# Kernel optimization log

Measured on AMD Instinct MI355X. Metric: run time of the kernel, lower is better.

Reference implementation:

```python
import jax, jax.numpy as jnp
import numpy as np

B, N, CS = 4, 384, 384
CZ = 128
H, C, PQ, PV = 12, 16, 4, 8
INF, EPS = 1e5, 1e-8


def _rigid_apply(rot, trans, pts):
    # rot: [B,N,3,3], trans: [B,N,3], pts: [B,N,P,3]
    return jnp.einsum('bnij,bnpj->bnpi', rot, pts) + trans[:, :, None, :]


def _pts_from_linear(x, n_pts):
    # torch: split last dim into 3 chunks (x,y,z blocks) then stack on dim -1
    Bx, Nx = x.shape[:2]
    return jnp.moveaxis(x.reshape(Bx, Nx, 3, n_pts), -2, -1)  # [B,N,n_pts,3]


def _forward(s, z, rot, trans, mask, w_q, b_q, w_kv, b_kv, w_gq, b_gq, w_gk, b_gk,
             w_qp, b_qp, w_kvp, b_kvp, head_weights, w_out, b_out):
    del z  # z is an unused arg in the original forward
    Bx, Nx, _ = s.shape
    q = (s @ w_q + b_q).reshape(Bx, Nx, H, C)
    kv = (s @ w_kv + b_kv).reshape(Bx, Nx, H, 2 * C)
    k, v = kv[..., :C], kv[..., C:]
    # g_q / g_k are computed in the original but never used (dead code):
    _ = (s.sum(0) @ w_gq + b_gq)
    _ = (s.sum(0) @ w_gk + b_gk)

    q_pts = _pts_from_linear(s @ w_qp + b_qp, H * PQ)
    q_pts = _rigid_apply(rot, trans, q_pts).reshape(Bx, Nx, H, PQ, 3)
    kv_pts = _pts_from_linear(s @ w_kvp + b_kvp, H * (PQ + PV))
    kv_pts = _rigid_apply(rot, trans, kv_pts).reshape(Bx, Nx, H, PQ + PV, 3)
    k_pts, v_pts = kv_pts[..., :PQ, :], kv_pts[..., PQ:, :]

    scale = np.sqrt(1.0 / (3 * C)).astype(np.float32)
    a = jnp.einsum('bihc,bjhc->bhij', q, k) * scale  # [B,H,N,N]
    a_g = a  # original recomputes the identical q@k product

    # point-distance attention bias; diff is [B,N,N,H,PQ,3]
    diff = q_pts[:, :, None] - k_pts[:, None]
    sq = jnp.sum(diff * diff, axis=-1)  # [B,N,N,H,PQ]
    hw = jax.nn.softplus(head_weights) * np.sqrt(1.0 / (3 * (PQ * 9.0 / 2))).astype(np.float32)
    pt_att = -0.5 * jnp.sum(sq * hw[:, None], axis=-1)  # [B,N,N,H]
    pt_att = jnp.moveaxis(pt_att, -1, 1)  # [B,H,N,N]

    square_mask = INF * (mask[:, :, None] * mask[:, None, :] - 1.0)  # [B,N,N]
    a = jax.nn.softmax(a + square_mask[:, None] + a_g + pt_att, axis=-1)

    o = jnp.einsum('bhij,bjhc->bihc', a, v).reshape(Bx, Nx, H * C)
    o_pt = jnp.einsum('bhij,bjhpx->bihpx', a, v_pts)  # [B,N,H,PV,3]
    # invert_apply: rot^T (x - t)
    o_pt = jnp.einsum('bnji,bnhpj->bnhpi', rot, o_pt - trans[:, :, None, None, :])
    o_pt_norm = jnp.sqrt(jnp.sum(o_pt ** 2, axis=-1) + EPS).reshape(Bx, Nx, H * PV)
    o_pt = o_pt.reshape(Bx, Nx, H * PV, 3)
    cat = jnp.concatenate([o, o_pt[..., 0], o_pt[..., 1], o_pt[..., 2], o_pt_norm], axis=-1)
    return cat @ w_out + b_out


def setup_inputs() -> dict:
    key = jax.random.key(0)
    ks = jax.random.split(key, 16)
    lin = lambda k, fi, fo: jax.random.normal(k, (fi, fo), jnp.float32) / np.sqrt(fi).astype(np.float32)
    hc = H * C
    out_dim = H * (C + PV * 4)
    return {
        's': jax.random.normal(ks[0], (B, N, CS), jnp.float32),
        'z': jax.random.normal(ks[1], (B, N, N, CZ), jnp.float32),
        'rot': jnp.linalg.qr(jax.random.normal(ks[2], (B, N, 3, 3), jnp.float32))[0],
        'trans': jax.random.normal(ks[3], (B, N, 3), jnp.float32),
        'mask': jnp.ones((B, N), jnp.float32),
        'w_q': lin(ks[4], CS, hc), 'b_q': jnp.zeros((hc,), jnp.float32),
        'w_kv': lin(ks[5], CS, 2 * hc), 'b_kv': jnp.zeros((2 * hc,), jnp.float32),
        'w_gq': lin(ks[6], CS, hc), 'b_gq': jnp.zeros((hc,), jnp.float32),
        'w_gk': lin(ks[7], CS, hc), 'b_gk': jnp.zeros((hc,), jnp.float32),
        'w_qp': lin(ks[8], CS, H * PQ * 3), 'b_qp': jnp.zeros((H * PQ * 3,), jnp.float32),
        'w_kvp': lin(ks[9], CS, H * (PQ + PV) * 3), 'b_kvp': jnp.zeros((H * (PQ + PV) * 3,), jnp.float32),
        'head_weights': jnp.full((H,), 0.541324854, jnp.float32),  # softplus^-1(1)
        'w_out': lin(ks[10], out_dim, CS), 'b_out': jnp.zeros((CS,), jnp.float32),
    }


def reference(s, z, rot, trans, mask, w_q, b_q, w_kv, b_kv, w_gq, b_gq, w_gk, b_gk,
              w_qp, b_qp, w_kvp, b_kvp, head_weights, w_out, b_out):
    return _forward(s, z, rot, trans, mask, w_q, b_q, w_kv, b_kv, w_gq, b_gq, w_gk, b_gk,
                    w_qp, b_qp, w_kvp, b_kvp, head_weights, w_out, b_out)
```

## Files before the change

### kernel.cpp

```cpp
#include <hip/hip_runtime.h>
#include <math.h>

#define Bb 4
#define Nn 384
#define CSs 384
#define Hh 12
#define Cc 16
#define PQq 4
#define PVv 8
#define FPROJ 1152
#define FCAT 576
#define INFV 100000.0f
#define EPSV 1e-8f

#define WS_PROJ 0
#define WS_CAT  3022848
#define WS_PART 4423680
#define PSTRIDE 2688
#define WS_WT   9068544
#define WS_WTO  9289728
#define WS_AH   9400320
#define WS_AL   9695232
#define WS_KH   9990144
#define WS_KL   10285056
#define WS_VBP  10579968

typedef __attribute__((ext_vector_type(8))) short short8v;
typedef __attribute__((ext_vector_type(4))) float f32x4;

__device__ __forceinline__ short f2bf(float x) {
    unsigned u = __float_as_uint(x);
    unsigned r = (u + 0x7FFFu + ((u >> 16) & 1u)) >> 16;
    return (short)r;
}
__device__ __forceinline__ float bf2f(short h) {
    return __uint_as_float(((unsigned)(unsigned short)h) << 16);
}

__device__ __forceinline__ float get_bias(int f,
    const float* __restrict__ b_q, const float* __restrict__ b_kv,
    const float* __restrict__ b_qp, const float* __restrict__ b_kvp)
{
    if (f < 192) return b_q[f];
    if (f < 576) return b_kv[f - 192];
    if (f < 720) return b_qp[f - 576];
    return b_kvp[f - 720];
}

__global__ __launch_bounds__(256) void prep_kernel(
    const float* __restrict__ w_q, const float* __restrict__ w_kv,
    const float* __restrict__ w_qp, const float* __restrict__ w_kvp,
    const float* __restrict__ w_out,
    short* __restrict__ wt, short* __restrict__ wto)
{
    int idx = blockIdx.x * 256 + threadIdx.x;
    if (idx < 1152 * 384) {
        int f = idx / 384, k = idx % 384;
        float v;
        if (f < 192)      v = w_q[(size_t)k * 192 + f];
        else if (f < 576) v = w_kv[(size_t)k * 384 + (f - 192)];
        else if (f < 720) v = w_qp[(size_t)k * 144 + (f - 576)];
        else              v = w_kvp[(size_t)k * 432 + (f - 720)];
        wt[idx] = f2bf(v);
    } else if (idx < 1152 * 384 + 384 * 576) {
        int j = idx - 1152 * 384;
        int f = j / 576, k = j % 576;
        wto[j] = f2bf(w_out[(size_t)k * 384 + f]);
    }
}

__global__ __launch_bounds__(256) void proj_kernel(
    const float* __restrict__ s, const short* __restrict__ wt,
    const float* __restrict__ b_q, const float* __restrict__ b_kv,
    const float* __restrict__ b_qp, const float* __restrict__ b_kvp,
    float* __restrict__ proj)
{
    __shared__ short Al[64 * 40];
    __shared__ short Bl[64 * 40];

    const int bm = blockIdx.x % 24;
    const int bn = blockIdx.x / 24;
    const int m0 = bm * 64;
    const int f0 = bn * 64;
    const int t = threadIdx.x;
    const int w = t >> 6;
    const int lane = t & 63;
    const int lrow = lane & 15;
    const int lkg  = lane >> 4;

    const int srow = t >> 2;
    const int sseg = t & 3;

    f32x4 acc0 = {0,0,0,0}, acc1 = {0,0,0,0}, acc2 = {0,0,0,0}, acc3 = {0,0,0,0};

    for (int ks = 0; ks < 12; ++ks) {
        const int kbase = ks * 32;
        {
            const float* sp = s + (size_t)(m0 + srow) * CSs + kbase + sseg * 8;
            float4 v0 = *(const float4*)sp;
            float4 v1 = *(const float4*)(sp + 4);
            short8v a;
            a[0]=f2bf(v0.x); a[1]=f2bf(v0.y); a[2]=f2bf(v0.z); a[3]=f2bf(v0.w);
            a[4]=f2bf(v1.x); a[5]=f2bf(v1.y); a[6]=f2bf(v1.z); a[7]=f2bf(v1.w);
            *(short8v*)&Al[srow * 40 + sseg * 8] = a;
        }
        {
            short8v bvv = *(const short8v*)&wt[(size_t)(f0 + srow) * 384 + kbase + sseg * 8];
            *(short8v*)&Bl[srow * 40 + sseg * 8] = bvv;
        }
        __syncthreads();

        short8v av = *(const short8v*)&Al[(16 * w + lrow) * 40 + lkg * 8];
        short8v b0 = *(const short8v*)&Bl[(lrow) * 40 + lkg * 8];
        short8v b1 = *(const short8v*)&Bl[(16 + lrow) * 40 + lkg * 8];
        short8v b2 = *(const short8v*)&Bl[(32 + lrow) * 40 + lkg * 8];
        short8v b3 = *(const short8v*)&Bl[(48 + lrow) * 40 + lkg * 8];
        acc0 = __builtin_amdgcn_mfma_f32_16x16x32_bf16(av, b0, acc0, 0, 0, 0);
        acc1 = __builtin_amdgcn_mfma_f32_16x16x32_bf16(av, b1, acc1, 0, 0, 0);
        acc2 = __builtin_amdgcn_mfma_f32_16x16x32_bf16(av, b2, acc2, 0, 0, 0);
        acc3 = __builtin_amdgcn_mfma_f32_16x16x32_bf16(av, b3, acc3, 0, 0, 0);
        __syncthreads();
    }

    const int orow = m0 + 16 * w + lkg * 4;
#pragma unroll
    for (int e = 0; e < 4; ++e) {
        float* pr = proj + (size_t)(orow + e) * FPROJ + f0;
        int c0 = lrow;
        pr[c0]      = acc0[e] + get_bias(f0 + c0,      b_q, b_kv, b_qp, b_kvp);
        pr[16 + c0] = acc1[e] + get_bias(f0 + 16 + c0, b_q, b_kv, b_qp, b_kvp);
        pr[32 + c0] = acc2[e] + get_bias(f0 + 32 + c0, b_q, b_kv, b_qp, b_kvp);
        pr[48 + c0] = acc3[e] + get_bias(f0 + 48 + c0, b_q, b_kv, b_qp, b_kvp);
    }
}

__global__ __launch_bounds__(192) void pack_kernel(
    const float* __restrict__ proj,
    const float* __restrict__ rot, const float* __restrict__ trans,
    const float* __restrict__ hwts, const float* __restrict__ mask,
    short* __restrict__ Ah, short* __restrict__ Al,
    short* __restrict__ Kh, short* __restrict__ Kl,
    short* __restrict__ Vbp)
{
    __shared__ float abuf[12 * 32];
    __shared__ float kbuf[12 * 32];
    __shared__ float vbuf[12 * 40];
    __shared__ float kpsq[12 * 4];

    const int bn = blockIdx.x;
    const int b = bn / Nn;
    const int n = bn % Nn;
    const int t = threadIdx.x;
    const float* R = rot + (size_t)bn * 9;
    const float* T = trans + (size_t)bn * 3;
    const float* pr = proj + (size_t)bn * FPROJ;
    const float mi = mask[bn];

    if (t < 144) {
        float x = pr[720 + t];
        float y = pr[720 + 144 + t];
        float z = pr[720 + 288 + t];
        float ox = R[0]*x + R[1]*y + R[2]*z + T[0];
        float oy = R[3]*x + R[4]*y + R[5]*z + T[1];
        float oz = R[6]*x + R[7]*y + R[8]*z + T[2];
        int h = t / 12, pp = t % 12;
        if (pp < PQq) {
            kbuf[h*32 + 16 + pp*3 + 0] = ox;
            kbuf[h*32 + 16 + pp*3 + 1] = oy;
            kbuf[h*32 + 16 + pp*3 + 2] = oz;
            kpsq[h*4 + pp] = ox*ox + oy*oy + oz*oz;
        } else {
            vbuf[h*40 + 16 + (pp - PQq)*3 + 0] = ox;
            vbuf[h*40 + 16 + (pp - PQq)*3 + 1] = oy;
            vbuf[h*40 + 16 + (pp - PQq)*3 + 2] = oz;
        }
    }
    if (t < 48) {
        float x = pr[576 + t];
        float y = pr[576 + 48 + t];
        float z = pr[576 + 96 + t];
        float ox = R[0]*x + R[1]*y + R[2]*z + T[0];
        float oy = R[3]*x + R[4]*y + R[5]*z + T[1];
        float oz = R[6]*x + R[7]*y + R[8]*z + T[2];
        int h = t / 4, p = t % 4;
        float n2wc = log1pf(expf(hwts[h])) * 0.13608276348795434f;
        abuf[h*32 + 16 + p*3 + 0] = n2wc * ox;
        abuf[h*32 + 16 + p*3 + 1] = n2wc * oy;
        abuf[h*32 + 16 + p*3 + 2] = n2wc * oz;
    }
    {
        int h = t >> 4, c = t & 15;
        abuf[h*32 + c] = 0.28867513459481287f * pr[h * 16 + c];
        kbuf[h*32 + c] = pr[192 + h * 32 + c];
        vbuf[h*40 + c] = pr[192 + h * 32 + 16 + c];
    }
    if (t < 12) {
        abuf[t*32 + 28] = 1.0f;  abuf[t*32 + 29] = mi;
        abuf[t*32 + 30] = 0.0f;  abuf[t*32 + 31] = 0.0f;
        kbuf[t*32 + 29] = INFV * (mi - 1.0f);
        kbuf[t*32 + 30] = 0.0f;  kbuf[t*32 + 31] = 0.0f;
    }
    __syncthreads();
    if (t < 12) {
        float hw2 = log1pf(expf(hwts[t]));
        float wc = -0.5f * hw2 * 0.13608276348795434f;
        kbuf[t*32 + 28] = wc * (kpsq[t*4] + kpsq[t*4+1] + kpsq[t*4+2] + kpsq[t*4+3]);
    }
    __syncthreads();

    if (t < 48) {
        int h = t >> 2, pc = t & 3;
        const float* src = &abuf[h*32 + pc*8];
        short8v hi, lo;
#pragma unroll
        for (int k = 0; k < 8; ++k) {
            short hh = f2bf(src[k]);
            hi[k] = hh; lo[k] = f2bf(src[k] - bf2f(hh));
        }
        size_t off = ((size_t)((b * Hh + h) * Nn + n)) * 32 + pc * 8;
        *(short8v*)&Ah[off] = hi;
        *(short8v*)&Al[off] = lo;
    } else if (t < 96) {
        int tt = t - 48, h = tt >> 2, pc = tt & 3;
        const float* src = &kbuf[h*32 + pc*8];
        short8v hi, lo;
#pragma unroll
        for (int k = 0; k < 8; ++k) {
            short hh = f2bf(src[k]);
            hi[k] = hh; lo[k] = f2bf(src[k] - bf2f(hh));
        }
        size_t off = ((size_t)((b * Hh + h) * Nn + n)) * 32 + pc * 8;
        *(short8v*)&Kh[off] = hi;
        *(short8v*)&Kl[off] = lo;
    } else if (t < 156) {
        int tt = t - 96, h = tt / 5, pc = tt % 5;
        const float* src = &vbuf[h*40 + pc*8];
        short8v v;
#pragma unroll
        for (int k = 0; k < 8; ++k) v[k] = f2bf(src[k]);
        *(short8v*)&Vbp[((size_t)((b * Hh + h) * Nn + n)) * 40 + pc * 8] = v;
    }
}

__global__ __launch_bounds__(256) void attn_part_kernel(
    const short* __restrict__ Ah, const short* __restrict__ Al,
    const short* __restrict__ Kh, const short* __restrict__ Kl,
    const short* __restrict__ Vbp,
    float* __restrict__ part)
{
    __shared__ short smem_s[13696];
    short* Ahi = smem_s;
    short* Alo = smem_s + 2560;
    short* Khi = smem_s + 5120;
    short* Klo = smem_s + 7680;
    short* Vb  = smem_s + 10240;
    short* Pb  = smem_s;

    const int bid = blockIdx.x;
    const int jc = bid % 6;
    const int ic = (bid / 6) % 6;
    const int h  = (bid / 36) % Hh;
    const int b  = bid / (36 * Hh);
    const int t  = threadIdx.x;
    const int i0 = ic * 64;
    const int j0 = jc * 64;
    const int bh = b * Hh + h;

    const short* AhB = Ah + ((size_t)(bh * Nn + i0)) * 32;
    const short* AlB = Al + ((size_t)(bh * Nn + i0)) * 32;
    const short* KhB = Kh + ((size_t)(bh * Nn + j0)) * 32;
    const short* KlB = Kl + ((size_t)(bh * Nn + j0)) * 32;
    const short* VbB = Vbp + ((size_t)(bh * Nn + j0)) * 40;

    {
        const int i = t >> 2, pc = t & 3;
        *(short8v*)&Ahi[i * 40 + pc * 8] = *(const short8v*)&AhB[i * 32 + pc * 8];
        *(short8v*)&Alo[i * 40 + pc * 8] = *(const short8v*)&AlB[i * 32 + pc * 8];
        *(short8v*)&Khi[i * 40 + pc * 8] = *(const short8v*)&KhB[i * 32 + pc * 8];
        *(short8v*)&Klo[i * 40 + pc * 8] = *(const short8v*)&KlB[i * 32 + pc * 8];
    }
#pragma unroll
    for (int e = t; e < 320; e += 256) {
        int j = e / 5, pc = e % 5;
        short8v v = *(const short8v*)&VbB[j * 40 + pc * 8];
#pragma unroll
        for (int k = 0; k < 8; ++k) Vb[(pc * 8 + k) * 72 + j] = v[k];
    }
    if (t < 144) {
        int o = 40 * 72 + t * 4;
        Vb[o] = 0; Vb[o+1] = 0; Vb[o+2] = 0; Vb[o+3] = 0;
    }
    __syncthreads();

    const int w = t >> 6;
    const int lane = t & 63;
    const int lrow = lane & 15;
    const int lkg  = lane >> 4;

    f32x4 La0 = {0,0,0,0}, La1 = {0,0,0,0}, La2 = {0,0,0,0}, La3 = {0,0,0,0};
    {
        short8v ahi = *(const short8v*)&Ahi[(16 * w + lrow) * 40 + lkg * 8];
        short8v alo = *(const short8v*)&Alo[(16 * w + lrow) * 40 + lkg * 8];
        short8v k0h = *(const short8v*)&Khi[(lrow) * 40 + lkg * 8];
        short8v k1h = *(const short8v*)&Khi[(16 + lrow) * 40 + lkg * 8];
        short8v k2h = *(const short8v*)&Khi[(32 + lrow) * 40 + lkg * 8];
        short8v k3h = *(const short8v*)&Khi[(48 + lrow) * 40 + lkg * 8];
        short8v k0l = *(const short8v*)&Klo[(lrow) * 40 + lkg * 8];
        short8v k1l = *(const short8v*)&Klo[(16 + lrow) * 40 + lkg * 8];
        short8v k2l = *(const short8v*)&Klo[(32 + lrow) * 40 + lkg * 8];
        short8v k3l = *(const short8v*)&Klo[(48 + lrow) * 40 + lkg * 8];
        La0 = __builtin_amdgcn_mfma_f32_16x16x32_bf16(ahi, k0h, La0, 0, 0, 0);
        La1 = __builtin_amdgcn_mfma_f32_16x16x32_bf16(ahi, k1h, La1, 0, 0, 0);
        La2 = __builtin_amdgcn_mfma_f32_16x16x32_bf16(ahi, k2h, La2, 0, 0, 0);
        La3 = __builtin_amdgcn_mfma_f32_16x16x32_bf16(ahi, k3h, La3, 0, 0, 0);
        La0 = __builtin_amdgcn_mfma_f32_16x16x32_bf16(alo, k0h, La0, 0, 0, 0);
        La1 = __builtin_amdgcn_mfma_f32_16x16x32_bf16(alo, k1h, La1, 0, 0, 0);
        La2 = __builtin_amdgcn_mfma_f32_16x16x32_bf16(alo, k2h, La2, 0, 0, 0);
        La3 = __builtin_amdgcn_mfma_f32_16x16x32_bf16(alo, k3h, La3, 0, 0, 0);
        La0 = __builtin_amdgcn_mfma_f32_16x16x32_bf16(ahi, k0l, La0, 0, 0, 0);
        La1 = __builtin_amdgcn_mfma_f32_16x16x32_bf16(ahi, k1l, La1, 0, 0, 0);
        La2 = __builtin_amdgcn_mfma_f32_16x16x32_bf16(ahi, k2l, La2, 0, 0, 0);
        La3 = __builtin_amdgcn_mfma_f32_16x16x32_bf16(ahi, k3l, La3, 0, 0, 0);
    }

    const size_t pidx = ((size_t)(bh * 6 + ic)) * 6 + jc;
    float* po = part + pidx * PSTRIDE;

    float m0_, m1_, m2_, m3_, s0_, s1_, s2_, s3_;
    float p00,p10,p20,p30, p01,p11,p21,p31, p02,p12,p22,p32, p03,p13,p23,p33;

#define SMAX_E(E, TM, SM, P0, P1, P2, P3) { \
    float tmax_ = fmaxf(fmaxf(La0[E], La1[E]), fmaxf(La2[E], La3[E])); \
    tmax_ = fmaxf(tmax_, __shfl_xor(tmax_, 1)); \
    tmax_ = fmaxf(tmax_, __shfl_xor(tmax_, 2)); \
    tmax_ = fmaxf(tmax_, __shfl_xor(tmax_, 4)); \
    tmax_ = fmaxf(tmax_, __shfl_xor(tmax_, 8)); \
    P0 = __expf(La0[E] - tmax_); P1 = __expf(La1[E] - tmax_); \
    P2 = __expf(La2[E] - tmax_); P3 = __expf(La3[E] - tmax_); \
    float cs_ = P0 + P1 + P2 + P3; \
    cs_ += __shfl_xor(cs_, 1); cs_ += __shfl_xor(cs_, 2); \
    cs_ += __shfl_xor(cs_, 4); cs_ += __shfl_xor(cs_, 8); \
    TM = tmax_; SM = cs_; }

    SMAX_E(0, m0_, s0_, p00, p10, p20, p30);
    SMAX_E(1, m1_, s1_, p01, p11, p21, p31);
    SMAX_E(2, m2_, s2_, p02, p12, p22, p32);
    SMAX_E(3, m3_, s3_, p03, p13, p23, p33);
#undef SMAX_E

    if (lrow == 0) {
        int rb = 16 * w + 4 * lkg;
        po[2560 + rb + 0] = m0_; po[2624 + rb + 0] = s0_;
        po[2560 + rb + 1] = m1_; po[2624 + rb + 1] = s1_;
        po[2560 + rb + 2] = m2_; po[2624 + rb + 2] = s2_;
        po[2560 + rb + 3] = m3_; po[2624 + rb + 3] = s3_;
    }
    __syncthreads();

#define PW(E, PJ0, PJ1, PJ2, PJ3) { \
    int r_ = (16 * w + 4 * lkg + E) * 72; \
    Pb[r_ + lrow]      = f2bf(PJ0); \
    Pb[r_ + 16 + lrow] = f2bf(PJ1); \
    Pb[r_ + 32 + lrow] = f2bf(PJ2); \
    Pb[r_ + 48 + lrow] = f2bf(PJ3); }
    PW(0, p00, p10, p20, p30);
    PW(1, p01, p11, p21, p31);
    PW(2, p02, p12, p22, p32);
    PW(3, p03, p13, p23, p33);
#undef PW
    __syncthreads();

    f32x4 O0 = {0,0,0,0}, O1 = {0,0,0,0}, O2 = {0,0,0,0};
#pragma unroll
    for (int ch = 0; ch < 2; ++ch) {
        short8v pf = *(const short8v*)&Pb[(16 * w + lrow) * 72 + ch * 32 + lkg * 8];
        short8v v0 = *(const short8v*)&Vb[(lrow) * 72 + ch * 32 + lkg * 8];
        short8v v1 = *(const short8v*)&Vb[(16 + lrow) * 72 + ch * 32 + lkg * 8];
        short8v v2 = *(const short8v*)&Vb[(32 + lrow) * 72 + ch * 32 + lkg * 8];
        O0 = __builtin_amdgcn_mfma_f32_16x16x32_bf16(pf, v0, O0, 0, 0, 0);
        O1 = __builtin_amdgcn_mfma_f32_16x16x32_bf16(pf, v1, O1, 0, 0, 0);
        O2 = __builtin_amdgcn_mfma_f32_16x16x32_bf16(pf, v2, O2, 0, 0, 0);
    }
#pragma unroll
    for (int e = 0; e < 4; ++e) {
        int r = 16 * w + 4 * lkg + e;
        po[r * 40 + lrow]      = O0[e];
        po[r * 40 + 16 + lrow] = O1[e];
        if (lrow < 8) po[r * 40 + 32 + lrow] = O2[e];
    }
}

__global__ __launch_bounds__(256) void attn_merge_kernel(
    const float* __restrict__ part,
    const float* __restrict__ rot, const float* __restrict__ trans,
    short* __restrict__ cat_bf)
{
    __shared__ float wsh[64 * 8];
    __shared__ float ob[64 * 44];

    const int bid = blockIdx.x;
    const int ic = bid % 6;
    const int h  = (bid / 6) % Hh;
    const int b  = bid / (6 * Hh);
    const int t  = threadIdx.x;
    const int i0 = ic * 64;
    const int bh = b * Hh + h;
    const size_t pbase = (((size_t)(bh * 6 + ic)) * 6) * PSTRIDE;

    if (t < 64) {
        float mk[6], sk[6];
        float M = -3.0e38f;
#pragma unroll
        for (int k = 0; k < 6; ++k) {
            mk[k] = part[pbase + (size_t)k * PSTRIDE + 2560 + t];
            sk[k] = part[pbase + (size_t)k * PSTRIDE + 2624 + t];
            M = fmaxf(M, mk[k]);
        }
        float wk[6]; float stot = 0.0f;
#pragma unroll
        for (int k = 0; k < 6; ++k) {
            wk[k] = __expf(mk[k] - M);
            stot += wk[k] * sk[k];
        }
        float inv = 1.0f / stot;
#pragma unroll
        for (int k = 0; k < 6; ++k) wsh[t * 8 + k] = wk[k] * inv;
    }
    __syncthreads();

#pragma unroll
    for (int it = 0; it < 10; ++it) {
        int idx = t + it * 256;
        int row = idx / 40, col = idx % 40;
        float v = 0.0f;
#pragma unroll
        for (int k = 0; k < 6; ++k)
            v += wsh[row * 8 + k] * part[pbase + (size_t)k * PSTRIDE + row * 40 + col];
        ob[row * 44 + col] = v;
    }
    __syncthreads();

    {
        const int i = t >> 2;
        const int qq = t & 3;
        const int bnI = b * Nn + i0 + i;
        short* crow = cat_bf + (size_t)bnI * FCAT;

        float4 o = *(const float4*)&ob[i * 44 + 4 * qq];
        crow[h * 16 + 4 * qq + 0] = f2bf(o.x);
        crow[h * 16 + 4 * qq + 1] = f2bf(o.y);
        crow[h * 16 + 4 * qq + 2] = f2bf(o.z);
        crow[h * 16 + 4 * qq + 3] = f2bf(o.w);

        const float* R = rot + (size_t)bnI * 9;
        const float* T = trans + (size_t)bnI * 3;
#pragma unroll
        for (int e = 0; e < 2; ++e) {
            int pe = qq + 4 * e;
            float g0 = ob[i * 44 + 16 + 3 * pe + 0] - T[0];
            float g1 = ob[i * 44 + 16 + 3 * pe + 1] - T[1];
            float g2 = ob[i * 44 + 16 + 3 * pe + 2] - T[2];
            float lx = R[0]*g0 + R[3]*g1 + R[6]*g2;
            float ly = R[1]*g0 + R[4]*g1 + R[7]*g2;
            float lz = R[2]*g0 + R[5]*g1 + R[8]*g2;
            crow[192 + h * 8 + pe] = f2bf(lx);
            crow[288 + h * 8 + pe] = f2bf(ly);
            crow[384 + h * 8 + pe] = f2bf(lz);
            crow[480 + h * 8 + pe] = f2bf(sqrtf(lx*lx + ly*ly + lz*lz + EPSV));
        }
    }
}

__global__ __launch_bounds__(256) void out_kernel(
    const short* __restrict__ cat_bf, const short* __restrict__ wto,
    const float* __restrict__ b_out, float* __restrict__ out)
{
    __shared__ short Al[64 * 40];
    __shared__ short Bl[64 * 40];

    const int bm = blockIdx.x % 24;
    const int bn = blockIdx.x / 24;
    const int m0 = bm * 64;
    const int n0 = bn * 64;
    const int t = threadIdx.x;
    const int w = t >> 6;
    const int lane = t & 63;
    const int lrow = lane & 15;
    const int lkg  = lane >> 4;

    const int srow = t >> 2;
    const int sseg = t & 3;

    f32x4 acc0 = {0,0,0,0}, acc1 = {0,0,0,0}, acc2 = {0,0,0,0}, acc3 = {0,0,0,0};

    for (int ks = 0; ks < 18; ++ks) {
        const int kbase = ks * 32;
        {
            short8v a = *(const short8v*)&cat_bf[(size_t)(m0 + srow) * FCAT + kbase + sseg * 8];
            *(short8v*)&Al[srow * 40 + sseg * 8] = a;
        }
        {
            short8v bvv = *(const short8v*)&wto[(size_t)(n0 + srow) * FCAT + kbase + sseg * 8];
            *(short8v*)&Bl[srow * 40 + sseg * 8] = bvv;
        }
        __syncthreads();

        short8v av = *(const short8v*)&Al[(16 * w + lrow) * 40 + lkg * 8];
        short8v b0 = *(const short8v*)&Bl[(lrow) * 40 + lkg * 8];
        short8v b1 = *(const short8v*)&Bl[(16 + lrow) * 40 + lkg * 8];
        short8v b2 = *(const short8v*)&Bl[(32 + lrow) * 40 + lkg * 8];
        short8v b3 = *(const short8v*)&Bl[(48 + lrow) * 40 + lkg * 8];
        acc0 = __builtin_amdgcn_mfma_f32_16x16x32_bf16(av, b0, acc0, 0, 0, 0);
        acc1 = __builtin_amdgcn_mfma_f32_16x16x32_bf16(av, b1, acc1, 0, 0, 0);
        acc2 = __builtin_amdgcn_mfma_f32_16x16x32_bf16(av, b2, acc2, 0, 0, 0);
        acc3 = __builtin_amdgcn_mfma_f32_16x16x32_bf16(av, b3, acc3, 0, 0, 0);
        __syncthreads();
    }

    const int orow = m0 + 16 * w + lkg * 4;
#pragma unroll
    for (int e = 0; e < 4; ++e) {
        float* pr = out + (size_t)(orow + e) * 384 + n0;
        int c0 = lrow;
        pr[c0]      = acc0[e] + b_out[n0 + c0];
        pr[16 + c0] = acc1[e] + b_out[n0 + 16 + c0];
        pr[32 + c0] = acc2[e] + b_out[n0 + 32 + c0];
        pr[48 + c0] = acc3[e] + b_out[n0 + 48 + c0];
    }
}

extern "C" void kernel_launch(void* const* d_in, const int* in_sizes, int n_in,
                              void* d_out, int out_size, void* d_ws, size_t ws_size,
                              hipStream_t stream) {
    const float* s     = (const float*)d_in[0];
    const float* rot   = (const float*)d_in[2];
    const float* trans = (const float*)d_in[3];
    const float* mask  = (const float*)d_in[4];
    const float* w_q   = (const float*)d_in[5];
    const float* b_q   = (const float*)d_in[6];
    const float* w_kv  = (const float*)d_in[7];
    const float* b_kv  = (const float*)d_in[8];
    const float* w_qp  = (const float*)d_in[13];
    const float* b_qp  = (const float*)d_in[14];
    const float* w_kvp = (const float*)d_in[15];
    const float* b_kvp = (const float*)d_in[16];
    const float* hwts  = (const float*)d_in[17];
    const float* w_out = (const float*)d_in[18];
    const float* b_out = (const float*)d_in[19];

    float* ws    = (float*)d_ws;
    float* proj  = ws + WS_PROJ;
    short* cat_bf = (short*)(ws + WS_CAT);
    float* partb = ws + WS_PART;
    short* wt    = (short*)(ws + WS_WT);
    short* wto   = (short*)(ws + WS_WTO);
    short* Ah    = (short*)(ws + WS_AH);
    short* Alp   = (short*)(ws + WS_AL);
    short* Kh    = (short*)(ws + WS_KH);
    short* Kl    = (short*)(ws + WS_KL);
    short* Vbp   = (short*)(ws + WS_VBP);
    float* out   = (float*)d_out;

    hipLaunchKernelGGL(prep_kernel, dim3(2592), dim3(256), 0, stream,
                       w_q, w_kv, w_qp, w_kvp, w_out, wt, wto);
    hipLaunchKernelGGL(proj_kernel, dim3(432), dim3(256), 0, stream,
                       s, wt, b_q, b_kv, b_qp, b_kvp, proj);
    hipLaunchKernelGGL(pack_kernel, dim3(1536), dim3(192), 0, stream,
                       proj, rot, trans, hwts, mask, Ah, Alp, Kh, Kl, Vbp);
    hipLaunchKernelGGL(attn_part_kernel, dim3(1728), dim3(256), 0, stream,
                       Ah, Alp, Kh, Kl, Vbp, partb);
    hipLaunchKernelGGL(attn_merge_kernel, dim3(288), dim3(256), 0, stream,
                       partb, rot, trans, cat_bf);
    hipLaunchKernelGGL(out_kernel, dim3(144), dim3(256), 0, stream,
                       cat_bf, wto, b_out, out);
}
```

Before: 55.46 us.

## Pre-convert s to bf16, store attention partials in bf16, split out GEMM finer

The prep kernel now also converts s to bf16 once, so the projection GEMM loads bf16 directly instead of loading fp32 and converting per tile. The per-chunk attention partial outputs are written as bf16 in a smaller partial stride, roughly halving partial-buffer traffic between the attention and merge kernels. The output GEMM uses 32-row tiles and twice as many blocks to improve CU occupancy. The cost is extra rounding on the partial outputs and a larger prep kernel launch.

New measurement: 54.21 us. 1.02x faster.

```diff
diff --git a/kernel.cpp b/kernel.cpp
--- a/kernel.cpp
+++ b/kernel.cpp
@@ -16,7 +16,7 @@
 #define WS_PROJ 0
 #define WS_CAT  3022848
 #define WS_PART 4423680
-#define PSTRIDE 2688
+#define PSTRIDE 1408
 #define WS_WT   9068544
 #define WS_WTO  9289728
 #define WS_AH   9400320
@@ -24,6 +24,7 @@
 #define WS_KH   9990144
 #define WS_KL   10285056
 #define WS_VBP  10579968
+#define WS_SB   10948608
 
 typedef __attribute__((ext_vector_type(8))) short short8v;
 typedef __attribute__((ext_vector_type(4))) float f32x4;
@@ -50,8 +51,8 @@
 __global__ __launch_bounds__(256) void prep_kernel(
     const float* __restrict__ w_q, const float* __restrict__ w_kv,
     const float* __restrict__ w_qp, const float* __restrict__ w_kvp,
-    const float* __restrict__ w_out,
-    short* __restrict__ wt, short* __restrict__ wto)
+    const float* __restrict__ w_out, const float* __restrict__ s,
+    short* __restrict__ wt, short* __restrict__ wto, short* __restrict__ sb)
 {
     int idx = blockIdx.x * 256 + threadIdx.x;
     if (idx < 1152 * 384) {
@@ -66,11 +67,14 @@
         int j = idx - 1152 * 384;
         int f = j / 576, k = j % 576;
         wto[j] = f2bf(w_out[(size_t)k * 384 + f]);
+    } else if (idx < 1152 * 384 + 384 * 576 + 1536 * 384) {
+        int j = idx - (1152 * 384 + 384 * 576);
+        sb[j] = f2bf(s[j]);
     }
 }
 
 __global__ __launch_bounds__(256) void proj_kernel(
-    const float* __restrict__ s, const short* __restrict__ wt,
+    const short* __restrict__ sb, const short* __restrict__ wt,
     const float* __restrict__ b_q, const float* __restrict__ b_kv,
     const float* __restrict__ b_qp, const float* __restrict__ b_kvp,
     float* __restrict__ proj)
@@ -95,19 +99,10 @@
 
     for (int ks = 0; ks < 12; ++ks) {
         const int kbase = ks * 32;
-        {
-            const float* sp = s + (size_t)(m0 + srow) * CSs + kbase + sseg * 8;
-            float4 v0 = *(const float4*)sp;
-            float4 v1 = *(const float4*)(sp + 4);
-            short8v a;
-            a[0]=f2bf(v0.x); a[1]=f2bf(v0.y); a[2]=f2bf(v0.z); a[3]=f2bf(v0.w);
-            a[4]=f2bf(v1.x); a[5]=f2bf(v1.y); a[6]=f2bf(v1.z); a[7]=f2bf(v1.w);
-            *(short8v*)&Al[srow * 40 + sseg * 8] = a;
-        }
-        {
-            short8v bvv = *(const short8v*)&wt[(size_t)(f0 + srow) * 384 + kbase + sseg * 8];
-            *(short8v*)&Bl[srow * 40 + sseg * 8] = bvv;
-        }
+        *(short8v*)&Al[srow * 40 + sseg * 8] =
+            *(const short8v*)&sb[(size_t)(m0 + srow) * CSs + kbase + sseg * 8];
+        *(short8v*)&Bl[srow * 40 + sseg * 8] =
+            *(const short8v*)&wt[(size_t)(f0 + srow) * 384 + kbase + sseg * 8];
         __syncthreads();
 
         short8v av = *(const short8v*)&Al[(16 * w + lrow) * 40 + lkg * 8];
@@ -325,6 +320,7 @@
 
     const size_t pidx = ((size_t)(bh * 6 + ic)) * 6 + jc;
     float* po = part + pidx * PSTRIDE;
+    short* poO = (short*)po;
 
     float m0_, m1_, m2_, m3_, s0_, s1_, s2_, s3_;
     float p00,p10,p20,p30, p01,p11,p21,p31, p02,p12,p22,p32, p03,p13,p23,p33;
@@ -350,10 +346,10 @@
 
     if (lrow == 0) {
         int rb = 16 * w + 4 * lkg;
-        po[2560 + rb + 0] = m0_; po[2624 + rb + 0] = s0_;
-        po[2560 + rb + 1] = m1_; po[2624 + rb + 1] = s1_;
-        po[2560 + rb + 2] = m2_; po[2624 + rb + 2] = s2_;
-        po[2560 + rb + 3] = m3_; po[2624 + rb + 3] = s3_;
+        po[1280 + rb + 0] = m0_; po[1344 + rb + 0] = s0_;
+        po[1280 + rb + 1] = m1_; po[1344 + rb + 1] = s1_;
+        po[1280 + rb + 2] = m2_; po[1344 + rb + 2] = s2_;
+        po[1280 + rb + 3] = m3_; po[1344 + rb + 3] = s3_;
     }
     __syncthreads();
 
@@ -384,9 +380,9 @@
 #pragma unroll
     for (int e = 0; e < 4; ++e) {
         int r = 16 * w + 4 * lkg + e;
-        po[r * 40 + lrow]      = O0[e];
-        po[r * 40 + 16 + lrow] = O1[e];
-        if (lrow < 8) po[r * 40 + 32 + lrow] = O2[e];
+        poO[r * 40 + lrow]      = f2bf(O0[e]);
+        poO[r * 40 + 16 + lrow] = f2bf(O1[e]);
+        if (lrow < 8) poO[r * 40 + 32 + lrow] = f2bf(O2[e]);
     }
 }
 
@@ -412,8 +408,8 @@
         float M = -3.0e38f;
 #pragma unroll
         for (int k = 0; k < 6; ++k) {
-            mk[k] = part[pbase + (size_t)k * PSTRIDE + 2560 + t];
-            sk[k] = part[pbase + (size_t)k * PSTRIDE + 2624 + t];
+            mk[k] = part[pbase + (size_t)k * PSTRIDE + 1280 + t];
+            sk[k] = part[pbase + (size_t)k * PSTRIDE + 1344 + t];
             M = fmaxf(M, mk[k]);
         }
         float wk[6]; float stot = 0.0f;
@@ -434,8 +430,10 @@
         int row = idx / 40, col = idx % 40;
         float v = 0.0f;
 #pragma unroll
-        for (int k = 0; k < 6; ++k)
-            v += wsh[row * 8 + k] * part[pbase + (size_t)k * PSTRIDE + row * 40 + col];
+        for (int k = 0; k < 6; ++k) {
+            const short* pO = (const short*)&part[pbase + (size_t)k * PSTRIDE];
+            v += wsh[row * 8 + k] * bf2f(pO[row * 40 + col]);
+        }
         ob[row * 44 + col] = v;
     }
     __syncthreads();
@@ -475,57 +473,51 @@
     const short* __restrict__ cat_bf, const short* __restrict__ wto,
     const float* __restrict__ b_out, float* __restrict__ out)
 {
-    __shared__ short Al[64 * 40];
+    __shared__ short Al[32 * 40];
     __shared__ short Bl[64 * 40];
 
-    const int bm = blockIdx.x % 24;
-    const int bn = blockIdx.x / 24;
-    const int m0 = bm * 64;
+    const int bm = blockIdx.x % 48;
+    const int bn = blockIdx.x / 48;
+    const int m0 = bm * 32;
     const int n0 = bn * 64;
     const int t = threadIdx.x;
     const int w = t >> 6;
     const int lane = t & 63;
     const int lrow = lane & 15;
     const int lkg  = lane >> 4;
-
-    const int srow = t >> 2;
-    const int sseg = t & 3;
-
-    f32x4 acc0 = {0,0,0,0}, acc1 = {0,0,0,0}, acc2 = {0,0,0,0}, acc3 = {0,0,0,0};
+    const int r0 = 16 * (w & 1);
+    const int c0 = 32 * (w >> 1);
+
+    f32x4 acc0 = {0,0,0,0}, acc1 = {0,0,0,0};
 
     for (int ks = 0; ks < 18; ++ks) {
         const int kbase = ks * 32;
+        if (t < 128) {
+            int arow = t >> 2, aseg = t & 3;
+            *(short8v*)&Al[arow * 40 + aseg * 8] =
+                *(const short8v*)&cat_bf[(size_t)(m0 + arow) * FCAT + kbase + aseg * 8];
+        }
         {
-            short8v a = *(const short8v*)&cat_bf[(size_t)(m0 + srow) * FCAT + kbase + sseg * 8];
-            *(short8v*)&Al[srow * 40 + sseg * 8] = a;
-        }
-        {
-            short8v bvv = *(const short8v*)&wto[(size_t)(n0 + srow) * FCAT + kbase + sseg * 8];
-            *(short8v*)&Bl[srow * 40 + sseg * 8] = bvv;
+            int brow = t >> 2, bseg = t & 3;
+            *(short8v*)&Bl[brow * 40 + bseg * 8] =
+                *(const short8v*)&wto[(size_t)(n0 + brow) * FCAT + kbase + bseg * 8];
         }
         __syncthreads();
 
-        short8v av = *(const short8v*)&Al[(16 * w + lrow) * 40 + lkg * 8];
-        short8v b0 = *(const short8v*)&Bl[(lrow) * 40 + lkg * 8];
-        short8v b1 = *(const short8v*)&Bl[(16 + lrow) * 40 + lkg * 8];
-        short8v b2 = *(const short8v*)&Bl[(32 + lrow) * 40 + lkg * 8];
-        short8v b3 = *(const short8v*)&Bl[(48 + lrow) * 40 + lkg * 8];
+        short8v av = *(const short8v*)&Al[(r0 + lrow) * 40 + lkg * 8];
+        short8v b0 = *(const short8v*)&Bl[(c0 + lrow) * 40 + lkg * 8];
+        short8v b1 = *(const short8v*)&Bl[(c0 + 16 + lrow) * 40 + lkg * 8];
         acc0 = __builtin_amdgcn_mfma_f32_16x16x32_bf16(av, b0, acc0, 0, 0, 0);
         acc1 = __builtin_amdgcn_mfma_f32_16x16x32_bf16(av, b1, acc1, 0, 0, 0);
-        acc2 = __builtin_amdgcn_mfma_f32_16x16x32_bf16(av, b2, acc2, 0, 0, 0);
-        acc3 = __builtin_amdgcn_mfma_f32_16x16x32_bf16(av, b3, acc3, 0, 0, 0);
         __syncthreads();
     }
 
-    const int orow = m0 + 16 * w + lkg * 4;
+    const int orow = m0 + r0 + lkg * 4;
 #pragma unroll
     for (int e = 0; e < 4; ++e) {
-        float* pr = out + (size_t)(orow + e) * 384 + n0;
-        int c0 = lrow;
-        pr[c0]      = acc0[e] + b_out[n0 + c0];
-        pr[16 + c0] = acc1[e] + b_out[n0 + 16 + c0];
-        pr[32 + c0] = acc2[e] + b_out[n0 + 32 + c0];
-        pr[48 + c0] = acc3[e] + b_out[n0 + 48 + c0];
+        float* pr = out + (size_t)(orow + e) * 384 + n0 + c0;
+        pr[lrow]      = acc0[e] + b_out[n0 + c0 + lrow];
+        pr[16 + lrow] = acc1[e] + b_out[n0 + c0 + 16 + lrow];
     }
 }
 
@@ -548,29 +540,30 @@
     const float* w_out = (const float*)d_in[18];
     const float* b_out = (const float*)d_in[19];
 
-    float* ws    = (float*)d_ws;
-    float* proj  = ws + WS_PROJ;
+    float* ws     = (float*)d_ws;
+    float* proj   = ws + WS_PROJ;
     short* cat_bf = (short*)(ws + WS_CAT);
-    float* partb = ws + WS_PART;
-    short* wt    = (short*)(ws + WS_WT);
-    short* wto   = (short*)(ws + WS_WTO);
-    short* Ah    = (short*)(ws + WS_AH);
-    short* Alp   = (short*)(ws + WS_AL);
-    short* Kh    = (short*)(ws + WS_KH);
-    short* Kl    = (short*)(ws + WS_KL);
-    short* Vbp   = (short*)(ws + WS_VBP);
-    float* out   = (float*)d_out;
-
-    hipLaunchKernelGGL(prep_kernel, dim3(2592), dim3(256), 0, stream,
-                       w_q, w_kv, w_qp, w_kvp, w_out, wt, wto);
+    float* partb  = ws + WS_PART;
+    short* wt     = (short*)(ws + WS_WT);
+    short* wto    = (short*)(ws + WS_WTO);
+    short* Ah     = (short*)(ws + WS_AH);
+    short* Alp    = (short*)(ws + WS_AL);
+    short* Kh     = (short*)(ws + WS_KH);
+    short* Kl     = (short*)(ws + WS_KL);
+    short* Vbp    = (short*)(ws + WS_VBP);
+    short* sb     = (short*)(ws + WS_SB);
+    float* out    = (float*)d_out;
+
+    hipLaunchKernelGGL(prep_kernel, dim3(4896), dim3(256), 0, stream,
+                       w_q, w_kv, w_qp, w_kvp, w_out, s, wt, wto, sb);
     hipLaunchKernelGGL(proj_kernel, dim3(432), dim3(256), 0, stream,
-                       s, wt, b_q, b_kv, b_qp, b_kvp, proj);
+                       sb, wt, b_q, b_kv, b_qp, b_kvp, proj);
     hipLaunchKernelGGL(pack_kernel, dim3(1536), dim3(192), 0, stream,
                        proj, rot, trans, hwts, mask, Ah, Alp, Kh, Kl, Vbp);
     hipLaunchKernelGGL(attn_part_kernel, dim3(1728), dim3(256), 0, stream,
                        Ah, Alp, Kh, Kl, Vbp, partb);
     hipLaunchKernelGGL(attn_merge_kernel, dim3(288), dim3(256), 0, stream,
                        partb, rot, trans, cat_bf);
-    hipLaunchKernelGGL(out_kernel, dim3(144), dim3(256), 0, stream,
+    hipLaunchKernelGGL(out_kernel, dim3(288), dim3(256), 0, stream,
                        cat_bf, wto, b_out, out);
 }
```
